# Kernel optimization log

Measured on AMD Instinct MI355X. Metric: run time of the kernel, lower is better.

## Reference

```python
import jax, jax.numpy as jnp
import numpy as np

VALUE_DECAY = 0.9
PENALTY_WEIGHT = 0.1
EPS = 1e-8


def setup_inputs() -> dict:
    key = jax.random.key(0)
    k1, k2, k3 = jax.random.split(key, 3)
    B, T, N, K, D = 16, 32, 6000, 32, 8
    preds = jax.random.normal(k1, (B, N, K), dtype=jnp.float32)
    y_ts = jax.random.normal(k2, (B, T, N, D), dtype=jnp.float32)
    importance = jax.random.uniform(k3, (D,), dtype=jnp.float32)
    return {"preds": preds, "y_ts": y_ts, "importance": importance}


def reference(preds, y_ts, importance):
    B, N, K = preds.shape
    _, T, _, D = y_ts.shape
    eye = jnp.eye(K, dtype=preds.dtype)

    # Batched ridge-regularized pseudo-inverse: (F^T F + eps I)^-1
    FtF = jnp.einsum('bnk,bnj->bkj', preds, preds)          # [B,K,K]
    inv_FtF = jnp.linalg.inv(FtF + EPS * eye)               # [B,K,K]

    Fty = jnp.einsum('bnk,btnd->btkd', preds, y_ts)         # [B,T,K,D]
    beta = jnp.einsum('bkj,btjd->btkd', inv_FtF, Fty)       # [B,T,K,D]
    y_hat = jnp.einsum('bnk,btkd->btnd', preds, beta)       # [B,T,N,D]

    ss_res = jnp.sum((y_ts - y_hat) ** 2, axis=2)           # [B,T,D]
    y_mean = jnp.mean(y_ts, axis=2, keepdims=True)          # [B,T,1,D]
    ss_tot = jnp.sum((y_ts - y_mean) ** 2, axis=2) + EPS    # [B,T,D]
    r2_d = 1.0 - ss_res / ss_tot                            # [B,T,D]
    weighted_r2 = jnp.einsum('btd,d->bt', r2_d, importance)  # [B,T]

    decay = VALUE_DECAY ** jnp.arange(T, dtype=preds.dtype)  # [T]
    total_r2 = jnp.sum(weighted_r2 * decay, axis=1)          # [B]
    loss_r2 = jnp.mean(-total_r2 / T)

    # Correlation penalty: corrcoef of the K factors over N samples, per batch
    Fc = preds - jnp.mean(preds, axis=1, keepdims=True)      # [B,N,K]
    cov = jnp.einsum('bnk,bnj->bkj', Fc, Fc)                 # [B,K,K] (scale cancels)
    std = jnp.sqrt(jnp.diagonal(cov, axis1=1, axis2=2))      # [B,K]
    corr = cov / (std[:, :, None] * std[:, None, :])         # [B,K,K]
    off = corr * (1.0 - eye)
    loss_corr = jnp.mean(jnp.sum(off ** 2, axis=(1, 2)))

    return loss_r2 + PENALTY_WEIGHT * loss_corr
```

## Files before the change

kernel.cpp:

```cpp
#include <hip/hip_runtime.h>

namespace {

constexpr int B_ = 16;
constexpr int T_ = 32;
constexpr int N_ = 6000;
constexpr int K_ = 32;
constexpr int D_ = 8;
constexpr float EPS_ = 1e-8f;
constexpr float PW_  = 0.1f;

constexpr int CH = 256;
constexpr int NB = 24;
constexpr int TS = 4;
constexpr int TC = T_ / TS;

constexpr int FTY_OFF = 0;
constexpr int SYY_OFF = FTY_OFF + B_*T_*K_*D_;
constexpr int SY_OFF  = SYY_OFF + B_*T_*D_;
constexpr int FTF_OFF = SY_OFF  + B_*T_*D_;
constexpr int SP_OFF  = FTF_OFF + B_*K_*K_;
constexpr int ZERO_FLOATS = SP_OFF + B_*K_;
constexpr int INV_OFF = ZERO_FLOATS;

__device__ inline void gload_lds16(const float* g, float* l) {
  __builtin_amdgcn_global_load_lds(
      (const __attribute__((address_space(1))) void*)g,
      (__attribute__((address_space(3))) void*)l, 16, 0, 0);
}

__global__ __launch_bounds__(512)
void stats_kernel(const float* __restrict__ preds,
                  const float* __restrict__ y,
                  float* __restrict__ ws)
{
  __shared__ float p_lds[CH * K_];
  __shared__ float y_lds[2][CH * D_];
  __shared__ float red[2][8 * 288];
  __shared__ float red2[2][8 * 16];

  const int tid  = threadIdx.x;
  const int w    = tid >> 6;
  const int lane = tid & 63;
  const int k    = lane & 31;
  const int nsub = lane >> 5;

  const int bid = blockIdx.x;
  const int ts  = bid & (TS - 1);
  const int c   = (bid >> 2) % NB;
  const int bb  = bid / (TS * NB);
  const int n0  = c * CH;
  const int rows_valid = min(CH, N_ - n0);
  const int t0  = ts * TC;

  const float* pb = preds + ((size_t)bb * N_ + n0) * K_;
  const int pvalid4 = rows_valid * 8;
  #pragma unroll
  for (int i = 0; i < 4; ++i) {
    const int idx = i * 512 + tid;
    if (idx < pvalid4) gload_lds16(pb + (size_t)idx * 4, p_lds + i * 2048 + w * 256);
    else *reinterpret_cast<float4*>(p_lds + idx * 4) = make_float4(0.f, 0.f, 0.f, 0.f);
  }

  const int yvalid4 = rows_valid * 2;
  {
    const float* src = y + (((size_t)bb * T_ + t0) * N_ + n0) * D_;
    if (tid < yvalid4) gload_lds16(src + (size_t)tid * 4, &y_lds[0][w * 256]);
    else *reinterpret_cast<float4*>(&y_lds[0][tid * 4]) = make_float4(0.f, 0.f, 0.f, 0.f);
  }

  __syncthreads();

  if (ts == 0) {
    float a2[K_];
    #pragma unroll
    for (int j = 0; j < K_; ++j) a2[j] = 0.f;
    float sp = 0.f;
    for (int it = 0; it < CH / 16; ++it) {
      const int nloc = it * 16 + w * 2 + nsub;
      const float pk = p_lds[nloc * K_ + k];
      sp += pk;
      const float4* row = reinterpret_cast<const float4*>(p_lds + nloc * K_);
      #pragma unroll
      for (int j4 = 0; j4 < 8; ++j4) {
        const float4 r = row[j4];
        a2[j4*4+0] = fmaf(pk, r.x, a2[j4*4+0]);
        a2[j4*4+1] = fmaf(pk, r.y, a2[j4*4+1]);
        a2[j4*4+2] = fmaf(pk, r.z, a2[j4*4+2]);
        a2[j4*4+3] = fmaf(pk, r.w, a2[j4*4+3]);
      }
    }
    #pragma unroll
    for (int j = 0; j < K_; ++j) a2[j] += __shfl_down(a2[j], 32);
    sp += __shfl_down(sp, 32);

    float* ftf = ws + FTF_OFF + bb * (K_*K_);
    #pragma unroll
    for (int g = 0; g < 4; ++g) {
      if (lane < 32) {
        #pragma unroll
        for (int j = 0; j < 8; ++j) red[0][w*288 + k*9 + j] = a2[g*8 + j];
      }
      __syncthreads();
      if (tid < 256) {
        const int kk = tid >> 3, jj = tid & 7;
        float s = 0.f;
        #pragma unroll
        for (int ww = 0; ww < 8; ++ww) s += red[0][ww*288 + kk*9 + jj];
        atomicAdd(&ftf[kk*K_ + g*8 + jj], s);
      }
      __syncthreads();
    }
    if (lane < 32) red[0][w*288 + k*9] = sp;
    __syncthreads();
    if (tid < 32) {
      float s = 0.f;
      #pragma unroll
      for (int ww = 0; ww < 8; ++ww) s += red[0][ww*288 + tid*9];
      atomicAdd(&ws[SP_OFF + bb*K_ + tid], s);
    }
    __syncthreads();
  }

  const int dly = lane & 7;
  const int q   = lane >> 3;
  const int itq = q >> 1;
  const int rq  = q & 1;

  int cur = 0;
  for (int tt = 0; tt < TC; ++tt) {
    const int t = t0 + tt;

    if (tt + 1 < TC) {
      const float* src = y + (((size_t)bb * T_ + (t + 1)) * N_ + n0) * D_;
      if (tid < yvalid4) gload_lds16(src + (size_t)tid * 4, &y_lds[cur ^ 1][w * 256]);
      else *reinterpret_cast<float4*>(&y_lds[cur ^ 1][tid * 4]) = make_float4(0.f, 0.f, 0.f, 0.f);
    }

    float acc[D_];
    #pragma unroll
    for (int d = 0; d < D_; ++d) acc[d] = 0.f;

    #pragma unroll 2
    for (int it = 0; it < 16; ++it) {
      const int nloc = it*16 + w*2 + nsub;
      const float pk = p_lds[nloc*K_ + k];
      const float4 y0 = *reinterpret_cast<const float4*>(&y_lds[cur][nloc*8]);
      const float4 y1 = *reinterpret_cast<const float4*>(&y_lds[cur][nloc*8 + 4]);
      acc[0] = fmaf(pk, y0.x, acc[0]);
      acc[1] = fmaf(pk, y0.y, acc[1]);
      acc[2] = fmaf(pk, y0.z, acc[2]);
      acc[3] = fmaf(pk, y0.w, acc[3]);
      acc[4] = fmaf(pk, y1.x, acc[4]);
      acc[5] = fmaf(pk, y1.y, acc[5]);
      acc[6] = fmaf(pk, y1.z, acc[6]);
      acc[7] = fmaf(pk, y1.w, acc[7]);
    }

    float syy = 0.f, sy = 0.f;
    #pragma unroll
    for (int j2 = 0; j2 < 4; ++j2) {
      const int it   = j2*4 + itq;
      const int nloc = it*16 + w*2 + rq;
      const float v = y_lds[cur][nloc*8 + dly];
      syy = fmaf(v, v, syy);
      sy += v;
    }

    #pragma unroll
    for (int d = 0; d < D_; ++d) acc[d] += __shfl_down(acc[d], 32);
    syy += __shfl_down(syy, 32);  sy += __shfl_down(sy, 32);
    syy += __shfl_down(syy, 16);  sy += __shfl_down(sy, 16);
    syy += __shfl_down(syy, 8);   sy += __shfl_down(sy, 8);

    const int par = tt & 1;
    if (lane < 32) {
      #pragma unroll
      for (int d = 0; d < D_; ++d) red[par][w*288 + k*9 + d] = acc[d];
    }
    if (lane < 8) { red2[par][w*16 + lane] = syy; red2[par][w*16 + 8 + lane] = sy; }
    __syncthreads();

    if (tid < 256) {
      const int kk = tid >> 3, dd = tid & 7;
      float s = 0.f;
      #pragma unroll
      for (int ww = 0; ww < 8; ++ww) s += red[par][ww*288 + kk*9 + dd];
      atomicAdd(&ws[FTY_OFF + ((size_t)(bb*T_ + t)*K_ + kk)*D_ + dd], s);
    } else if (tid < 272) {
      const int i2  = tid - 256;
      const int dd  = i2 & 7;
      const int sel = i2 >> 3;
      float s = 0.f;
      #pragma unroll
      for (int ww = 0; ww < 8; ++ww) s += red2[par][ww*16 + sel*8 + dd];
      atomicAdd(&ws[(sel ? SY_OFF : SYY_OFF) + (bb*T_ + t)*D_ + dd], s);
    }
    cur ^= 1;
  }
}

__global__ __launch_bounds__(64)
void invert_kernel(float* __restrict__ ws)
{
  const int b = blockIdx.x;
  const int lane = threadIdx.x;
  const float* A = ws + FTF_OFF + b * (K_*K_);

  float m[32];
  #pragma unroll
  for (int r = 0; r < 32; ++r) {
    if (lane < 32) m[r] = A[r*32 + lane] + (r == lane ? EPS_ : 0.f);
    else           m[r] = ((lane - 32) == r) ? 1.f : 0.f;
  }

  #pragma unroll
  for (int p = 0; p < 32; ++p) {
    const float ip = 1.0f / __shfl(m[p], p);
    m[p] *= ip;
    #pragma unroll
    for (int r = 0; r < 32; ++r) {
      if (r == p) continue;
      const float f = __shfl(m[r], p);
      m[r] = fmaf(-f, m[p], m[r]);
    }
  }

  float* out = ws + INV_OFF + b * (K_*K_);
  #pragma unroll
  for (int r = 0; r < 32; ++r)
    if (lane >= 32) out[r*32 + (lane - 32)] = m[r];
}

__global__ __launch_bounds__(256)
void finish_kernel(const float* __restrict__ ws,
                   const float* __restrict__ imp,
                   float* __restrict__ out)
{
  const int bt = blockIdx.x;
  const int b  = bt / T_;
  const int t  = bt - b * T_;
  const int tid = threadIdx.x;

  __shared__ float sInv[32][33];
  __shared__ float sFty[256];
  __shared__ float sRed[32][8];
  __shared__ float sW[8];

  for (int idx = tid; idx < 1024; idx += 256)
    sInv[idx >> 5][idx & 31] = ws[INV_OFF + b*(K_*K_) + idx];
  sFty[tid] = ws[FTY_OFF + (size_t)bt * 256 + tid];
  __syncthreads();

  const int kk = tid >> 3, dd = tid & 7;
  float beta = 0.f;
  #pragma unroll
  for (int j = 0; j < 32; ++j) beta = fmaf(sInv[kk][j], sFty[j*8 + dd], beta);
  const float fty = sFty[kk*8 + dd];
  sRed[kk][dd] = fty * beta + EPS_ * beta * beta;
  __syncthreads();

  if (tid < 8) {
    float dots = 0.f;
    #pragma unroll
    for (int k2 = 0; k2 < 32; ++k2) dots += sRed[k2][tid];
    const float syy = ws[SYY_OFF + bt*D_ + tid];
    const float syv = ws[SY_OFF  + bt*D_ + tid];
    const float ss_res = syy - dots;
    const float ss_tot = syy - syv*syv*(1.0f/N_) + EPS_;
    sW[tid] = (1.f - ss_res/ss_tot) * imp[tid];
  }
  __syncthreads();

  if (tid == 0) {
    float wr2 = 0.f;
    #pragma unroll
    for (int d = 0; d < 8; ++d) wr2 += sW[d];
    atomicAdd(out, -wr2 * powf(0.9f, (float)t) * (1.0f / (T_ * B_)));
  }
}

__global__ __launch_bounds__(256)
void corr_kernel(const float* __restrict__ ws, float* __restrict__ out)
{
  const int b = blockIdx.x;
  const int tid = threadIdx.x;
  __shared__ float sC[32][33];
  __shared__ float sStd[32];

  for (int idx = tid; idx < 1024; idx += 256) {
    const int r = idx >> 5, c2 = idx & 31;
    const float cov = ws[FTF_OFF + b*(K_*K_) + idx]
                    - ws[SP_OFF + b*K_ + r] * ws[SP_OFF + b*K_ + c2] * (1.0f/N_);
    sC[r][c2] = cov;
  }
  __syncthreads();
  if (tid < 32) sStd[tid] = sqrtf(sC[tid][tid]);
  __syncthreads();

  float acc = 0.f;
  for (int idx = tid; idx < 1024; idx += 256) {
    const int r = idx >> 5, c2 = idx & 31;
    if (r != c2) {
      const float cr = sC[r][c2] / (sStd[r] * sStd[c2]);
      acc = fmaf(cr, cr, acc);
    }
  }
  acc += __shfl_down(acc, 32);
  acc += __shfl_down(acc, 16);
  acc += __shfl_down(acc, 8);
  acc += __shfl_down(acc, 4);
  acc += __shfl_down(acc, 2);
  acc += __shfl_down(acc, 1);
  if ((tid & 63) == 0) atomicAdd(out, acc * (PW_ / B_));
}

}

extern "C" void kernel_launch(void* const* d_in, const int* in_sizes, int n_in,
                              void* d_out, int out_size, void* d_ws, size_t ws_size,
                              hipStream_t stream)
{
  const float* preds = (const float*)d_in[0];
  const float* y     = (const float*)d_in[1];
  const float* imp   = (const float*)d_in[2];
  float* out = (float*)d_out;
  float* ws  = (float*)d_ws;

  hipMemsetAsync(ws, 0, (size_t)ZERO_FLOATS * sizeof(float), stream);
  hipMemsetAsync(out, 0, sizeof(float), stream);

  stats_kernel<<<B_ * NB * TS, 512, 0, stream>>>(preds, y, ws);
  invert_kernel<<<B_, 64, 0, stream>>>(ws);
  finish_kernel<<<B_ * T_, 256, 0, stream>>>(ws, imp, out);
  corr_kernel<<<B_, 256, 0, stream>>>(ws, out);
}
```

Baseline: 239.5 us.

## Compute F^T y with bf16 MFMA, one wave per timestep, preload all y tiles

Reworks the stats kernel so each of the 8 waves owns one timestep. All of the block's y tiles are loaded into LDS up front instead of double-buffered per timestep. The F^T y partial products now use bf16 16x16x32 MFMA instructions with per-wave atomics directly to global, removing the per-timestep block reductions and barriers. The cost is precision: preds and y are rounded to bf16, which may shift the R2 loss. Half of the MFMA B-columns are padding zeros, and LDS use grows.

```diff
diff --git a/kernel.cpp b/kernel.cpp
--- a/kernel.cpp
+++ b/kernel.cpp
@@ -23,6 +23,15 @@
 constexpr int ZERO_FLOATS = SP_OFF + B_*K_;
 constexpr int INV_OFF = ZERO_FLOATS;
 
+typedef short  bf16x8 __attribute__((ext_vector_type(8)));
+typedef float  f32x4  __attribute__((ext_vector_type(4)));
+
+__device__ inline short f2bf(float v) {
+  unsigned u = __float_as_uint(v);
+  unsigned r = (u + 0x7fffu + ((u >> 16) & 1u)) >> 16;
+  return (short)r;
+}
+
 __device__ inline void gload_lds16(const float* g, float* l) {
   __builtin_amdgcn_global_load_lds(
       (const __attribute__((address_space(1))) void*)g,
@@ -35,15 +44,12 @@
                   float* __restrict__ ws)
 {
   __shared__ float p_lds[CH * K_];
-  __shared__ float y_lds[2][CH * D_];
-  __shared__ float red[2][8 * 288];
-  __shared__ float red2[2][8 * 16];
+  __shared__ float y_lds[TC][CH * D_];
+  __shared__ float red[8 * 288];
 
   const int tid  = threadIdx.x;
   const int w    = tid >> 6;
   const int lane = tid & 63;
-  const int k    = lane & 31;
-  const int nsub = lane >> 5;
 
   const int bid = blockIdx.x;
   const int ts  = bid & (TS - 1);
@@ -62,16 +68,22 @@
     else *reinterpret_cast<float4*>(p_lds + idx * 4) = make_float4(0.f, 0.f, 0.f, 0.f);
   }
 
+  const int t = t0 + w;
+  float* slot = &y_lds[w][0];
   const int yvalid4 = rows_valid * 2;
-  {
-    const float* src = y + (((size_t)bb * T_ + t0) * N_ + n0) * D_;
-    if (tid < yvalid4) gload_lds16(src + (size_t)tid * 4, &y_lds[0][w * 256]);
-    else *reinterpret_cast<float4*>(&y_lds[0][tid * 4]) = make_float4(0.f, 0.f, 0.f, 0.f);
+  const float* ysrc = y + (((size_t)bb * T_ + t) * N_ + n0) * D_;
+  #pragma unroll
+  for (int i = 0; i < 8; ++i) {
+    const int idx4 = i * 64 + lane;
+    if (idx4 < yvalid4) gload_lds16(ysrc + (size_t)idx4 * 4, slot + i * 256);
+    else *reinterpret_cast<float4*>(slot + idx4 * 4) = make_float4(0.f, 0.f, 0.f, 0.f);
   }
 
   __syncthreads();
 
   if (ts == 0) {
+    const int k    = lane & 31;
+    const int nsub = lane >> 5;
     float a2[K_];
     #pragma unroll
     for (int j = 0; j < K_; ++j) a2[j] = 0.f;
@@ -99,104 +111,78 @@
     for (int g = 0; g < 4; ++g) {
       if (lane < 32) {
         #pragma unroll
-        for (int j = 0; j < 8; ++j) red[0][w*288 + k*9 + j] = a2[g*8 + j];
+        for (int j = 0; j < 8; ++j) red[w*288 + k*9 + j] = a2[g*8 + j];
       }
       __syncthreads();
       if (tid < 256) {
         const int kk = tid >> 3, jj = tid & 7;
         float s = 0.f;
         #pragma unroll
-        for (int ww = 0; ww < 8; ++ww) s += red[0][ww*288 + kk*9 + jj];
+        for (int ww = 0; ww < 8; ++ww) s += red[ww*288 + kk*9 + jj];
         atomicAdd(&ftf[kk*K_ + g*8 + jj], s);
       }
       __syncthreads();
     }
-    if (lane < 32) red[0][w*288 + k*9] = sp;
+    if (lane < 32) red[w*288 + k*9] = sp;
     __syncthreads();
     if (tid < 32) {
       float s = 0.f;
       #pragma unroll
-      for (int ww = 0; ww < 8; ++ww) s += red[0][ww*288 + tid*9];
+      for (int ww = 0; ww < 8; ++ww) s += red[ww*288 + tid*9];
       atomicAdd(&ws[SP_OFF + bb*K_ + tid], s);
     }
-    __syncthreads();
-  }
-
-  const int dly = lane & 7;
-  const int q   = lane >> 3;
-  const int itq = q >> 1;
-  const int rq  = q & 1;
-
-  int cur = 0;
-  for (int tt = 0; tt < TC; ++tt) {
-    const int t = t0 + tt;
-
-    if (tt + 1 < TC) {
-      const float* src = y + (((size_t)bb * T_ + (t + 1)) * N_ + n0) * D_;
-      if (tid < yvalid4) gload_lds16(src + (size_t)tid * 4, &y_lds[cur ^ 1][w * 256]);
-      else *reinterpret_cast<float4*>(&y_lds[cur ^ 1][tid * 4]) = make_float4(0.f, 0.f, 0.f, 0.f);
-    }
-
-    float acc[D_];
-    #pragma unroll
-    for (int d = 0; d < D_; ++d) acc[d] = 0.f;
-
-    #pragma unroll 2
-    for (int it = 0; it < 16; ++it) {
-      const int nloc = it*16 + w*2 + nsub;
-      const float pk = p_lds[nloc*K_ + k];
-      const float4 y0 = *reinterpret_cast<const float4*>(&y_lds[cur][nloc*8]);
-      const float4 y1 = *reinterpret_cast<const float4*>(&y_lds[cur][nloc*8 + 4]);
-      acc[0] = fmaf(pk, y0.x, acc[0]);
-      acc[1] = fmaf(pk, y0.y, acc[1]);
-      acc[2] = fmaf(pk, y0.z, acc[2]);
-      acc[3] = fmaf(pk, y0.w, acc[3]);
-      acc[4] = fmaf(pk, y1.x, acc[4]);
-      acc[5] = fmaf(pk, y1.y, acc[5]);
-      acc[6] = fmaf(pk, y1.z, acc[6]);
-      acc[7] = fmaf(pk, y1.w, acc[7]);
-    }
-
-    float syy = 0.f, sy = 0.f;
-    #pragma unroll
-    for (int j2 = 0; j2 < 4; ++j2) {
-      const int it   = j2*4 + itq;
-      const int nloc = it*16 + w*2 + rq;
-      const float v = y_lds[cur][nloc*8 + dly];
+  }
+
+  const int mrow = lane & 15;
+  const int g8   = (lane >> 4) * 8;
+  bf16x8 afrag[8][2];
+  #pragma unroll
+  for (int nt = 0; nt < 8; ++nt) {
+    #pragma unroll
+    for (int mt = 0; mt < 2; ++mt) {
+      bf16x8 f;
+      #pragma unroll
+      for (int j = 0; j < 8; ++j)
+        f[j] = f2bf(p_lds[(nt*32 + g8 + j) * K_ + mt*16 + mrow]);
+      afrag[nt][mt] = f;
+    }
+  }
+
+  const int dcol = lane & 15;
+  const bool dok = dcol < 8;
+  f32x4 acc0 = {0.f, 0.f, 0.f, 0.f};
+  f32x4 acc1 = {0.f, 0.f, 0.f, 0.f};
+  float syy = 0.f, sy = 0.f;
+
+  #pragma unroll
+  for (int nt = 0; nt < 8; ++nt) {
+    bf16x8 bfr;
+    #pragma unroll
+    for (int j = 0; j < 8; ++j) {
+      const float v = dok ? slot[(nt*32 + g8 + j) * D_ + dcol] : 0.f;
       syy = fmaf(v, v, syy);
       sy += v;
-    }
-
-    #pragma unroll
-    for (int d = 0; d < D_; ++d) acc[d] += __shfl_down(acc[d], 32);
-    syy += __shfl_down(syy, 32);  sy += __shfl_down(sy, 32);
-    syy += __shfl_down(syy, 16);  sy += __shfl_down(sy, 16);
-    syy += __shfl_down(syy, 8);   sy += __shfl_down(sy, 8);
-
-    const int par = tt & 1;
-    if (lane < 32) {
-      #pragma unroll
-      for (int d = 0; d < D_; ++d) red[par][w*288 + k*9 + d] = acc[d];
-    }
-    if (lane < 8) { red2[par][w*16 + lane] = syy; red2[par][w*16 + 8 + lane] = sy; }
-    __syncthreads();
-
-    if (tid < 256) {
-      const int kk = tid >> 3, dd = tid & 7;
-      float s = 0.f;
-      #pragma unroll
-      for (int ww = 0; ww < 8; ++ww) s += red[par][ww*288 + kk*9 + dd];
-      atomicAdd(&ws[FTY_OFF + ((size_t)(bb*T_ + t)*K_ + kk)*D_ + dd], s);
-    } else if (tid < 272) {
-      const int i2  = tid - 256;
-      const int dd  = i2 & 7;
-      const int sel = i2 >> 3;
-      float s = 0.f;
-      #pragma unroll
-      for (int ww = 0; ww < 8; ++ww) s += red2[par][ww*16 + sel*8 + dd];
-      atomicAdd(&ws[(sel ? SY_OFF : SYY_OFF) + (bb*T_ + t)*D_ + dd], s);
-    }
-    cur ^= 1;
+      bfr[j] = f2bf(v);
+    }
+    acc0 = __builtin_amdgcn_mfma_f32_16x16x32_bf16(afrag[nt][0], bfr, acc0, 0, 0, 0);
+    acc1 = __builtin_amdgcn_mfma_f32_16x16x32_bf16(afrag[nt][1], bfr, acc1, 0, 0, 0);
+  }
+
+  syy += __shfl_down(syy, 32);  sy += __shfl_down(sy, 32);
+  syy += __shfl_down(syy, 16);  sy += __shfl_down(sy, 16);
+  if (lane < 8) {
+    atomicAdd(&ws[SYY_OFF + ((size_t)bb*T_ + t)*D_ + lane], syy);
+    atomicAdd(&ws[SY_OFF  + ((size_t)bb*T_ + t)*D_ + lane], sy);
+  }
+
+  if (dok) {
+    float* fty = ws + FTY_OFF + (size_t)(bb*T_ + t) * (K_*D_);
+    #pragma unroll
+    for (int r = 0; r < 4; ++r) {
+      const int row = (lane >> 4) * 4 + r;
+      atomicAdd(&fty[row        * D_ + dcol], acc0[r]);
+      atomicAdd(&fty[(16 + row) * D_ + dcol], acc1[r]);
+    }
   }
 }
 
```

New measurement: 241.5 us. Within noise of the previous version (+0.8%).
